# Performance work log

Hardware: AMD Instinct MI355X
Metric: run time of the kernel (lower is better)

## Reference

```python
import jax, jax.numpy as jnp
import numpy as np
from jax import lax

D_MODEL = 384
D_INNER = 768   # expand * d_model
D_STATE = 16
DT_RANK = 24
K_CONV = 4
B_SZ = 2
L_SEQ = 2048


def setup_inputs() -> dict:
    key = jax.random.key(0)
    ks = jax.random.split(key, 11)
    inp = {}
    inp["x"] = jax.random.normal(ks[0], (B_SZ, L_SEQ, D_MODEL), dtype=jnp.float32)
    # learned parameters (Mamba block)
    inp["in_proj_w"] = jax.random.normal(ks[1], (D_MODEL, 2 * D_INNER), dtype=jnp.float32) * 0.02
    inp["conv_w"] = jax.random.normal(ks[2], (D_INNER, K_CONV), dtype=jnp.float32) * 0.1
    inp["conv_b"] = jnp.zeros((D_INNER,), dtype=jnp.float32)
    inp["x_proj_w"] = jax.random.normal(ks[3], (D_INNER, DT_RANK + 2 * D_STATE), dtype=jnp.float32) * 0.02
    inp["dt_proj_w"] = jax.random.normal(ks[4], (DT_RANK, D_INNER), dtype=jnp.float32) * 0.1
    inp["dt_proj_b"] = jnp.full((D_INNER,), -2.0, dtype=jnp.float32)  # softplus(-2) ~ small init dt
    # A_log initialized so A = -exp(A_log) = -[1..d_state]
    inp["A_log"] = jnp.log(jnp.broadcast_to(jnp.arange(1, D_STATE + 1, dtype=jnp.float32), (D_INNER, D_STATE)))
    inp["D"] = jnp.ones((D_INNER,), dtype=jnp.float32)
    inp["out_proj_w"] = jax.random.normal(ks[5], (D_INNER, D_MODEL), dtype=jnp.float32) * 0.02
    return inp


def _silu(x):
    return x * jax.nn.sigmoid(x)


def reference(x, in_proj_w, conv_w, conv_b, x_proj_w, dt_proj_w, dt_proj_b, A_log, D, out_proj_w):
    B, L, _ = x.shape
    d_inner, n = A_log.shape
    k = conv_w.shape[-1]

    # input projection and gate split
    xz = jnp.einsum("bld,de->ble", x, in_proj_w)          # [B, L, 2*d_inner]
    xp, z = jnp.split(xz, 2, axis=-1)                       # each [B, L, d_inner]

    # causal depthwise 1D conv along sequence
    xp_t = xp.transpose(0, 2, 1)                            # [B, d_inner, L]
    conv_out = lax.conv_general_dilated(
        xp_t, conv_w[:, None, :],                           # kernel [O=d_inner, I/g=1, K]
        window_strides=(1,), padding=[(k - 1, 0)],
        dimension_numbers=("NCH", "OIH", "NCH"),
        feature_group_count=d_inner,
    ) + conv_b[None, :, None]
    xp = _silu(conv_out.transpose(0, 2, 1))                 # [B, L, d_inner]

    # data-dependent SSM parameters
    x_dbl = jnp.einsum("bld,de->ble", xp, x_proj_w)         # [B, L, dt_rank + 2n]
    dt_r = x_dbl[..., :DT_RANK]
    Bm = x_dbl[..., DT_RANK:DT_RANK + n]                    # [B, L, n]
    Cm = x_dbl[..., DT_RANK + n:]                           # [B, L, n]
    dt = jax.nn.softplus(jnp.einsum("blr,rd->bld", dt_r, dt_proj_w) + dt_proj_b)  # [B, L, d_inner]

    A = -jnp.exp(A_log)                                     # [d_inner, n]
    dA = jnp.exp(jnp.einsum("bld,dn->bldn", dt, A))         # discretized state transition
    dBx = jnp.einsum("bln,bld->bldn", Bm, dt * xp)          # input contribution

    # sequential selective scan over L
    def step(h, inputs):
        dA_t, dBx_t, C_t = inputs                           # [B,d,n],[B,d,n],[B,n]
        h = dA_t * h + dBx_t
        y = jnp.einsum("bdn,bn->bd", h, C_t)
        return h, y

    h0 = jnp.zeros((B, d_inner, n), dtype=x.dtype)
    _, ys = lax.scan(step, h0, (dA.transpose(1, 0, 2, 3), dBx.transpose(1, 0, 2, 3), Cm.transpose(1, 0, 2)))
    y = ys.transpose(1, 0, 2)                               # [B, L, d_inner]

    y = y + xp * D                                          # skip term
    y = y * _silu(z)                                        # gating
    return jnp.einsum("bld,de->ble", y, out_proj_w)         # [B, L, d_model]
```

## Files before the change

kernel.cpp:

```cpp
#include <hip/hip_runtime.h>
#include <hip/hip_bf16.h>

#define B_SZ    2
#define L_SEQ   2048
#define D_MODEL 384
#define D_INNER 768
#define D_STATE 16
#define DT_RANK 24
#define ML      (B_SZ * L_SEQ)
#define NCHUNK  64
#define CHLEN   (L_SEQ / NCHUNK)

typedef __hip_bfloat16 bf16;
typedef __attribute__((ext_vector_type(8))) short bf16x8;
typedef __attribute__((ext_vector_type(4))) float f32x4;
typedef __attribute__((ext_vector_type(8))) float f32x8;

template<int EPI, int AMODE>
__global__ __launch_bounds__(256)
void gemm_mfma(const float* __restrict__ Af, const bf16* __restrict__ At,
               const float* __restrict__ W,
               bf16* __restrict__ outb0, bf16* __restrict__ outb1,
               float* __restrict__ outf, int M, int N, int K)
{
    __shared__ __attribute__((aligned(16))) short As[64][72];
    __shared__ __attribute__((aligned(16))) short Bs[64][72];
    const int tid  = threadIdx.x;
    const int lane = tid & 63;
    const int wave = tid >> 6;
    const int wm   = (wave & 1) * 32;
    const int wn   = (wave >> 1) * 32;
    const int m0   = blockIdx.y * 64;
    const int n0   = blockIdx.x * 64;

    f32x4 acc[2][2];
#pragma unroll
    for (int i = 0; i < 2; i++)
#pragma unroll
        for (int j = 0; j < 2; j++)
#pragma unroll
            for (int r = 0; r < 4; r++) acc[i][j][r] = 0.f;

    for (int kt = 0; kt < K; kt += 64) {
        __syncthreads();
#pragma unroll
        for (int i = 0; i < 2; i++) {
            int c = tid + 256 * i;
            if (AMODE == 0) {
                int m = c >> 3, k8 = (c & 7) * 8;
                f32x8 a = *(const f32x8*)&Af[(size_t)(m0 + m) * K + kt + k8];
                bf16x8 h;
#pragma unroll
                for (int j = 0; j < 8; j++)
                    h[j] = (short)__bfloat16_as_ushort(__float2bfloat16(a[j]));
                *(bf16x8*)&As[m][k8] = h;
            } else {
                int m8 = (c & 7) * 8, k = c >> 3;
                bf16x8 a = *(const bf16x8*)&At[(size_t)(kt + k) * M + m0 + m8];
#pragma unroll
                for (int j = 0; j < 8; j++) As[m8 + j][k] = a[j];
            }
        }
#pragma unroll
        for (int i = 0; i < 2; i++) {
            int c = tid + 256 * i;
            int n8 = (c & 7) * 8, k = c >> 3;
            if (n0 + n8 + 8 <= N) {
                f32x8 w = *(const f32x8*)&W[(size_t)(kt + k) * N + n0 + n8];
#pragma unroll
                for (int j = 0; j < 8; j++)
                    Bs[n8 + j][k] = (short)__bfloat16_as_ushort(__float2bfloat16(w[j]));
            } else {
#pragma unroll
                for (int j = 0; j < 8; j++) Bs[n8 + j][k] = 0;
            }
        }
        __syncthreads();
#pragma unroll
        for (int ks = 0; ks < 2; ks++) {
            int kb = ks * 32 + (lane >> 4) * 8;
            bf16x8 a0 = *(const bf16x8*)&As[wm + (lane & 15)][kb];
            bf16x8 a1 = *(const bf16x8*)&As[wm + 16 + (lane & 15)][kb];
            bf16x8 b0 = *(const bf16x8*)&Bs[wn + (lane & 15)][kb];
            bf16x8 b1 = *(const bf16x8*)&Bs[wn + 16 + (lane & 15)][kb];
            acc[0][0] = __builtin_amdgcn_mfma_f32_16x16x32_bf16(a0, b0, acc[0][0], 0, 0, 0);
            acc[0][1] = __builtin_amdgcn_mfma_f32_16x16x32_bf16(a0, b1, acc[0][1], 0, 0, 0);
            acc[1][0] = __builtin_amdgcn_mfma_f32_16x16x32_bf16(a1, b0, acc[1][0], 0, 0, 0);
            acc[1][1] = __builtin_amdgcn_mfma_f32_16x16x32_bf16(a1, b1, acc[1][1], 0, 0, 0);
        }
    }

#pragma unroll
    for (int am = 0; am < 2; am++)
#pragma unroll
        for (int bn = 0; bn < 2; bn++)
#pragma unroll
            for (int r = 0; r < 4; r++) {
                int m = m0 + wm + am * 16 + (lane >> 4) * 4 + r;
                int n = n0 + wn + bn * 16 + (lane & 15);
                float v = acc[am][bn][r];
                if (EPI == 0) {
                    if (n < D_INNER)
                        outb0[(size_t)n * ML + m] = __float2bfloat16(v);
                    else
                        outb1[(size_t)(n - D_INNER) * ML + m] =
                            __float2bfloat16(v / (1.f + __expf(-v)));
                } else {
                    if (n < N) outf[(size_t)m * N + n] = v;
                }
            }
}

__global__ __launch_bounds__(256)
void gemm_xproj_split(const bf16* __restrict__ At, const float* __restrict__ W,
                      float* __restrict__ outf, int M, int N, int K)
{
    __shared__ __attribute__((aligned(16))) short As[64][72];
    __shared__ __attribute__((aligned(16))) short Bs[64][72];
    const int tid  = threadIdx.x;
    const int lane = tid & 63;
    const int wave = tid >> 6;
    const int wm   = (wave & 1) * 32;
    const int wn   = (wave >> 1) * 32;
    const int m0   = blockIdx.y * 64;
    const int k0   = blockIdx.x * (768 / 4);

    f32x4 acc[2][2];
#pragma unroll
    for (int i = 0; i < 2; i++)
#pragma unroll
        for (int j = 0; j < 2; j++)
#pragma unroll
            for (int r = 0; r < 4; r++) acc[i][j][r] = 0.f;

    for (int kt = k0; kt < k0 + 192; kt += 64) {
        __syncthreads();
#pragma unroll
        for (int i = 0; i < 2; i++) {
            int c = tid + 256 * i;
            int m8 = (c & 7) * 8, k = c >> 3;
            bf16x8 a = *(const bf16x8*)&At[(size_t)(kt + k) * M + m0 + m8];
#pragma unroll
            for (int j = 0; j < 8; j++) As[m8 + j][k] = a[j];
        }
#pragma unroll
        for (int i = 0; i < 2; i++) {
            int c = tid + 256 * i;
            int n8 = (c & 7) * 8, k = c >> 3;
            if (n8 + 8 <= N) {
                f32x8 w = *(const f32x8*)&W[(size_t)(kt + k) * N + n8];
#pragma unroll
                for (int j = 0; j < 8; j++)
                    Bs[n8 + j][k] = (short)__bfloat16_as_ushort(__float2bfloat16(w[j]));
            } else {
#pragma unroll
                for (int j = 0; j < 8; j++) Bs[n8 + j][k] = 0;
            }
        }
        __syncthreads();
#pragma unroll
        for (int ks = 0; ks < 2; ks++) {
            int kb = ks * 32 + (lane >> 4) * 8;
            bf16x8 a0 = *(const bf16x8*)&As[wm + (lane & 15)][kb];
            bf16x8 a1 = *(const bf16x8*)&As[wm + 16 + (lane & 15)][kb];
            bf16x8 b0 = *(const bf16x8*)&Bs[wn + (lane & 15)][kb];
            bf16x8 b1 = *(const bf16x8*)&Bs[wn + 16 + (lane & 15)][kb];
            acc[0][0] = __builtin_amdgcn_mfma_f32_16x16x32_bf16(a0, b0, acc[0][0], 0, 0, 0);
            acc[0][1] = __builtin_amdgcn_mfma_f32_16x16x32_bf16(a0, b1, acc[0][1], 0, 0, 0);
            acc[1][0] = __builtin_amdgcn_mfma_f32_16x16x32_bf16(a1, b0, acc[1][0], 0, 0, 0);
            acc[1][1] = __builtin_amdgcn_mfma_f32_16x16x32_bf16(a1, b1, acc[1][1], 0, 0, 0);
        }
    }

#pragma unroll
    for (int am = 0; am < 2; am++)
#pragma unroll
        for (int bn = 0; bn < 2; bn++)
#pragma unroll
            for (int r = 0; r < 4; r++) {
                int m = m0 + wm + am * 16 + (lane >> 4) * 4 + r;
                int n = wn + bn * 16 + (lane & 15);
                if (n < N)
                    atomicAdd(&outf[(size_t)m * N + n], acc[am][bn][r]);
            }
}

__global__ __launch_bounds__(256)
void conv_silu_kernel(const bf16* __restrict__ xp_raw_t,
                      const float* __restrict__ cw, const float* __restrict__ cb,
                      bf16* __restrict__ xp_t, float* __restrict__ x_dbl_zero)
{
    {
        int gidx = (blockIdx.y * gridDim.x + blockIdx.x) * 256 + threadIdx.x;
        if (gidx < ML * 56) x_dbl_zero[gidx] = 0.f;
    }

    const int ml0 = (blockIdx.x * 256 + threadIdx.x) * 8;
    const int d   = blockIdx.y;
    const int l0  = ml0 & (L_SEQ - 1);
    const size_t row = (size_t)d * ML;
    const float w0 = cw[d * 4 + 0], w1 = cw[d * 4 + 1],
                w2 = cw[d * 4 + 2], w3 = cw[d * 4 + 3], bias = cb[d];

    bf16x8 cur = *(const bf16x8*)&xp_raw_t[row + ml0];
    bf16x8 prev;
    if (ml0 != 0) prev = *(const bf16x8*)&xp_raw_t[row + ml0 - 8];
    else {
#pragma unroll
        for (int j = 0; j < 8; j++) prev[j] = 0;
    }
    float w[16];
#pragma unroll
    for (int k = 0; k < 8; k++) {
        w[k]     = __uint_as_float(((unsigned)(unsigned short)prev[k]) << 16);
        w[k + 8] = __uint_as_float(((unsigned)(unsigned short)cur[k]) << 16);
    }

    bf16x8 out;
#pragma unroll
    for (int o = 0; o < 8; o++) {
        int l = l0 + o;
        float s = bias;
        if (l >= 3) {
            s += w0 * w[5 + o] + w1 * w[6 + o] + w2 * w[7 + o] + w3 * w[8 + o];
        } else {
            if (l - 3 >= 0) s += w0 * w[5 + o];
            if (l - 2 >= 0) s += w1 * w[6 + o];
            if (l - 1 >= 0) s += w2 * w[7 + o];
            s += w3 * w[8 + o];
        }
        float act = s / (1.f + __expf(-s));
        out[o] = (short)__bfloat16_as_ushort(__float2bfloat16(act));
    }
    *(bf16x8*)&xp_t[row + ml0] = out;
}

__global__ __launch_bounds__(256)
void dt_kernel(const float* __restrict__ x_dbl, const float* __restrict__ dtw,
               const float* __restrict__ dtb, bf16* __restrict__ dt_t)
{
    __shared__ float xs[64 * 25];
    __shared__ float ws[24 * 48];
    const int tid = threadIdx.x;
    const int m0 = blockIdx.x * 64;
    const int d0 = blockIdx.y * 48;
#pragma unroll
    for (int i = 0; i < 6; i++) {
        int idx = tid + 256 * i;
        int r_ = idx / 24, cc = idx % 24;
        xs[r_ * 25 + cc] = x_dbl[(size_t)(m0 + r_) * 56 + cc];
    }
#pragma unroll
    for (int i = 0; i < 5; i++) {
        int idx = tid + 256 * i;
        if (idx < 24 * 48) {
            int r_ = idx / 48, dd = idx % 48;
            ws[idx] = dtw[r_ * D_INNER + d0 + dd];
        }
    }
    __syncthreads();
#pragma unroll
    for (int i = 0; i < 12; i++) {
        int o = tid + 256 * i;
        int mloc = o & 63, dd = o >> 6;
        float acc = dtb[d0 + dd];
#pragma unroll
        for (int r_ = 0; r_ < 24; r_++)
            acc += xs[mloc * 25 + r_] * ws[r_ * 48 + dd];
        float sp = fmaxf(acc, 0.f) + log1pf(__expf(-fabsf(acc)));
        dt_t[(size_t)(d0 + dd) * ML + m0 + mloc] = __float2bfloat16(sp);
    }
}

__global__ __launch_bounds__(1024)
void scan_kernel(const bf16* __restrict__ dt_t, const bf16* __restrict__ xp_t,
                 const float* __restrict__ x_dbl, const bf16* __restrict__ zs_t,
                 const float* __restrict__ A_log, const float* __restrict__ Dp,
                 bf16* __restrict__ y_t)
{
    __shared__ float sP[NCHUNK][D_STATE + 1];
    __shared__ float sH[NCHUNK][D_STATE + 1];
    const int tid = threadIdx.x;
    const int c = tid >> 4;
    const int n = tid & 15;
    const int g = blockIdx.x;
    const int b = g / D_INNER;
    const int d = g % D_INNER;
    const float A = -__expf(A_log[d * D_STATE + n]);
    const size_t base_t = (size_t)d * ML + (size_t)b * L_SEQ + (size_t)c * CHLEN;
    const size_t base_m = (size_t)b * L_SEQ + (size_t)c * CHLEN;

    float h = 0.f, P = 1.f;
#pragma unroll
    for (int g2 = 0; g2 < 2; g2++) {
        bf16x8 vdt0 = *(const bf16x8*)&dt_t[base_t + g2 * 16];
        bf16x8 vdt1 = *(const bf16x8*)&dt_t[base_t + g2 * 16 + 8];
        bf16x8 vxp0 = *(const bf16x8*)&xp_t[base_t + g2 * 16];
        bf16x8 vxp1 = *(const bf16x8*)&xp_t[base_t + g2 * 16 + 8];
#pragma unroll
        for (int k = 0; k < 16; k++) {
            const int j = g2 * 16 + k;
            short sdt = (k < 8) ? vdt0[k & 7] : vdt1[k & 7];
            short sxp = (k < 8) ? vxp0[k & 7] : vxp1[k & 7];
            float dtv = __uint_as_float(((unsigned)(unsigned short)sdt) << 16);
            float xpv = __uint_as_float(((unsigned)(unsigned short)sxp) << 16);
            float Bn  = x_dbl[(base_m + j) * 56 + DT_RANK + n];
            float aj = __expf(dtv * A);
            h = aj * h + Bn * (dtv * xpv);
            P *= aj;
        }
    }
    sP[c][n] = P;
    sH[c][n] = h;
    __syncthreads();

    {
        const int wv = tid >> 6;
        const int ln = tid & 63;
        float p = sP[ln][wv];
        float hh = sH[ln][wv];
#pragma unroll
        for (int s = 1; s < NCHUNK; s <<= 1) {
            float p2 = __shfl_up(p, s);
            float h2 = __shfl_up(hh, s);
            if (ln >= s) { hh = p * h2 + hh; p = p * p2; }
        }
        sP[ln][wv] = p;
        sH[ln][wv] = hh;
    }
    __syncthreads();
    const float hinit = (c == 0) ? 0.f : sH[c - 1][n];

    const float Dd = Dp[d];
    h = hinit;
#pragma unroll
    for (int g2 = 0; g2 < 2; g2++) {
        bf16x8 vdt0 = *(const bf16x8*)&dt_t[base_t + g2 * 16];
        bf16x8 vdt1 = *(const bf16x8*)&dt_t[base_t + g2 * 16 + 8];
        bf16x8 vxp0 = *(const bf16x8*)&xp_t[base_t + g2 * 16];
        bf16x8 vxp1 = *(const bf16x8*)&xp_t[base_t + g2 * 16 + 8];
        float ymine = 0.f, xmine = 0.f;
#pragma unroll
        for (int k = 0; k < 16; k++) {
            const int j = g2 * 16 + k;
            short sdt = (k < 8) ? vdt0[k & 7] : vdt1[k & 7];
            short sxp = (k < 8) ? vxp0[k & 7] : vxp1[k & 7];
            float dtv = __uint_as_float(((unsigned)(unsigned short)sdt) << 16);
            float xpv = __uint_as_float(((unsigned)(unsigned short)sxp) << 16);
            float Bn  = x_dbl[(base_m + j) * 56 + DT_RANK + n];
            float aj = __expf(dtv * A);
            h = aj * h + Bn * (dtv * xpv);
            float Cn = x_dbl[(base_m + j) * 56 + DT_RANK + D_STATE + n];
            float yv = h * Cn;
            yv += __shfl_xor(yv, 1);
            yv += __shfl_xor(yv, 2);
            yv += __shfl_xor(yv, 4);
            yv += __shfl_xor(yv, 8);
            ymine = (k == n) ? yv : ymine;
            xmine = (k == n) ? xpv : xmine;
        }
        const int j = g2 * 16 + n;
        float zsv = __bfloat162float(zs_t[base_t + j]);
        y_t[base_t + j] = __float2bfloat16((ymine + xmine * Dd) * zsv);
    }
}

extern "C" void kernel_launch(void* const* d_in, const int* in_sizes, int n_in,
                              void* d_out, int out_size, void* d_ws, size_t ws_size,
                              hipStream_t stream)
{
    const float* x         = (const float*)d_in[0];
    const float* in_proj_w = (const float*)d_in[1];
    const float* conv_w    = (const float*)d_in[2];
    const float* conv_b    = (const float*)d_in[3];
    const float* x_proj_w  = (const float*)d_in[4];
    const float* dt_proj_w = (const float*)d_in[5];
    const float* dt_proj_b = (const float*)d_in[6];
    const float* A_log     = (const float*)d_in[7];
    const float* Dvec      = (const float*)d_in[8];
    const float* out_proj_w= (const float*)d_in[9];

    bf16* xp_raw_t = (bf16*)d_ws;
    bf16* zs_t     = xp_raw_t + (size_t)ML * D_INNER;
    bf16* xp_t     = zs_t     + (size_t)ML * D_INNER;
    bf16* dt_t     = xp_t     + (size_t)ML * D_INNER;
    float* x_dbl   = (float*)(dt_t + (size_t)ML * D_INNER);
    bf16* y_t      = xp_raw_t;

    dim3 blk(256);

    gemm_mfma<0, 0><<<dim3(2 * D_INNER / 64, ML / 64), blk, 0, stream>>>(
        x, nullptr, in_proj_w, xp_raw_t, zs_t, nullptr, ML, 2 * D_INNER, D_MODEL);

    conv_silu_kernel<<<dim3(ML / 2048, D_INNER), blk, 0, stream>>>(
        xp_raw_t, conv_w, conv_b, xp_t, x_dbl);

    gemm_xproj_split<<<dim3(4, ML / 64), blk, 0, stream>>>(
        xp_t, x_proj_w, x_dbl, ML, 56, D_INNER);

    dt_kernel<<<dim3(ML / 64, D_INNER / 48), blk, 0, stream>>>(
        x_dbl, dt_proj_w, dt_proj_b, dt_t);

    scan_kernel<<<B_SZ * D_INNER, 1024, 0, stream>>>(
        dt_t, xp_t, x_dbl, zs_t, A_log, Dvec, y_t);

    gemm_mfma<1, 1><<<dim3(D_MODEL / 64, ML / 64), blk, 0, stream>>>(
        nullptr, y_t, out_proj_w, nullptr, nullptr, (float*)d_out, ML, D_MODEL, D_INNER);
}
```

Baseline: 239.8 us.

## Store B/C state-major and reuse first-pass scan results instead of recomputing

The x_proj epilogue now writes dt_rank values to a compact row-major buffer and the B and C columns to a transposed [n][ML] buffer, so the scan can load B and C with contiguous vector loads. The scan's first pass keeps per-step h*C and P*C in registers. The second pass then computes outputs as hC + hinit*(P*C) instead of re-running the recurrence with exp and reloading inputs. This removes the redundant second recurrence and the strided per-element x_dbl loads. In exchange it uses 64 extra registers per thread in a 1024-thread block, which risks spills or lower occupancy.

```diff
diff --git a/kernel.cpp b/kernel.cpp
--- a/kernel.cpp
+++ b/kernel.cpp
@@ -113,7 +113,8 @@
 
 __global__ __launch_bounds__(256)
 void gemm_xproj_split(const bf16* __restrict__ At, const float* __restrict__ W,
-                      float* __restrict__ outf, int M, int N, int K)
+                      float* __restrict__ out_dt, float* __restrict__ out_bc,
+                      int M, int N, int K)
 {
     __shared__ __attribute__((aligned(16))) short As[64][72];
     __shared__ __attribute__((aligned(16))) short Bs[64][72];
@@ -180,8 +181,11 @@
             for (int r = 0; r < 4; r++) {
                 int m = m0 + wm + am * 16 + (lane >> 4) * 4 + r;
                 int n = wn + bn * 16 + (lane & 15);
-                if (n < N)
-                    atomicAdd(&outf[(size_t)m * N + n], acc[am][bn][r]);
+                float v = acc[am][bn][r];
+                if (n < DT_RANK)
+                    atomicAdd(&out_dt[(size_t)m * DT_RANK + n], v);
+                else if (n < DT_RANK + 2 * D_STATE)
+                    atomicAdd(&out_bc[(size_t)(n - DT_RANK) * ML + m], v);
             }
 }
 
@@ -248,7 +252,7 @@
     for (int i = 0; i < 6; i++) {
         int idx = tid + 256 * i;
         int r_ = idx / 24, cc = idx % 24;
-        xs[r_ * 25 + cc] = x_dbl[(size_t)(m0 + r_) * 56 + cc];
+        xs[r_ * 25 + cc] = x_dbl[(size_t)(m0 + r_) * 24 + cc];
     }
 #pragma unroll
     for (int i = 0; i < 5; i++) {
@@ -274,7 +278,7 @@
 
 __global__ __launch_bounds__(1024)
 void scan_kernel(const bf16* __restrict__ dt_t, const bf16* __restrict__ xp_t,
-                 const float* __restrict__ x_dbl, const bf16* __restrict__ zs_t,
+                 const float* __restrict__ bc, const bf16* __restrict__ zs_t,
                  const float* __restrict__ A_log, const float* __restrict__ Dp,
                  bf16* __restrict__ y_t)
 {
@@ -289,25 +293,31 @@
     const float A = -__expf(A_log[d * D_STATE + n]);
     const size_t base_t = (size_t)d * ML + (size_t)b * L_SEQ + (size_t)c * CHLEN;
     const size_t base_m = (size_t)b * L_SEQ + (size_t)c * CHLEN;
-
+    const float* __restrict__ Bp = bc + (size_t)n * ML + base_m;
+    const float* __restrict__ Cp = bc + (size_t)(D_STATE + n) * ML + base_m;
+
+    float hC[CHLEN], sc[CHLEN];
     float h = 0.f, P = 1.f;
 #pragma unroll
-    for (int g2 = 0; g2 < 2; g2++) {
-        bf16x8 vdt0 = *(const bf16x8*)&dt_t[base_t + g2 * 16];
-        bf16x8 vdt1 = *(const bf16x8*)&dt_t[base_t + g2 * 16 + 8];
-        bf16x8 vxp0 = *(const bf16x8*)&xp_t[base_t + g2 * 16];
-        bf16x8 vxp1 = *(const bf16x8*)&xp_t[base_t + g2 * 16 + 8];
-#pragma unroll
-        for (int k = 0; k < 16; k++) {
-            const int j = g2 * 16 + k;
-            short sdt = (k < 8) ? vdt0[k & 7] : vdt1[k & 7];
-            short sxp = (k < 8) ? vxp0[k & 7] : vxp1[k & 7];
-            float dtv = __uint_as_float(((unsigned)(unsigned short)sdt) << 16);
-            float xpv = __uint_as_float(((unsigned)(unsigned short)sxp) << 16);
-            float Bn  = x_dbl[(base_m + j) * 56 + DT_RANK + n];
+    for (int q = 0; q < 4; q++) {
+        bf16x8 vdt = *(const bf16x8*)&dt_t[base_t + q * 8];
+        bf16x8 vxp = *(const bf16x8*)&xp_t[base_t + q * 8];
+        f32x4 b0 = *(const f32x4*)&Bp[q * 8];
+        f32x4 b1 = *(const f32x4*)&Bp[q * 8 + 4];
+        f32x4 c0 = *(const f32x4*)&Cp[q * 8];
+        f32x4 c1 = *(const f32x4*)&Cp[q * 8 + 4];
+#pragma unroll
+        for (int k = 0; k < 8; k++) {
+            const int j = q * 8 + k;
+            float dtv = __uint_as_float(((unsigned)(unsigned short)vdt[k]) << 16);
+            float xpv = __uint_as_float(((unsigned)(unsigned short)vxp[k]) << 16);
+            float Bn  = (k < 4) ? b0[k & 3] : b1[k & 3];
+            float Cn  = (k < 4) ? c0[k & 3] : c1[k & 3];
             float aj = __expf(dtv * A);
             h = aj * h + Bn * (dtv * xpv);
             P *= aj;
+            hC[j] = h * Cn;
+            sc[j] = P * Cn;
         }
     }
     sP[c][n] = P;
@@ -332,36 +342,23 @@
     const float hinit = (c == 0) ? 0.f : sH[c - 1][n];
 
     const float Dd = Dp[d];
-    h = hinit;
 #pragma unroll
     for (int g2 = 0; g2 < 2; g2++) {
-        bf16x8 vdt0 = *(const bf16x8*)&dt_t[base_t + g2 * 16];
-        bf16x8 vdt1 = *(const bf16x8*)&dt_t[base_t + g2 * 16 + 8];
-        bf16x8 vxp0 = *(const bf16x8*)&xp_t[base_t + g2 * 16];
-        bf16x8 vxp1 = *(const bf16x8*)&xp_t[base_t + g2 * 16 + 8];
-        float ymine = 0.f, xmine = 0.f;
+        float ymine = 0.f;
 #pragma unroll
         for (int k = 0; k < 16; k++) {
             const int j = g2 * 16 + k;
-            short sdt = (k < 8) ? vdt0[k & 7] : vdt1[k & 7];
-            short sxp = (k < 8) ? vxp0[k & 7] : vxp1[k & 7];
-            float dtv = __uint_as_float(((unsigned)(unsigned short)sdt) << 16);
-            float xpv = __uint_as_float(((unsigned)(unsigned short)sxp) << 16);
-            float Bn  = x_dbl[(base_m + j) * 56 + DT_RANK + n];
-            float aj = __expf(dtv * A);
-            h = aj * h + Bn * (dtv * xpv);
-            float Cn = x_dbl[(base_m + j) * 56 + DT_RANK + D_STATE + n];
-            float yv = h * Cn;
-            yv += __shfl_xor(yv, 1);
-            yv += __shfl_xor(yv, 2);
-            yv += __shfl_xor(yv, 4);
-            yv += __shfl_xor(yv, 8);
-            ymine = (k == n) ? yv : ymine;
-            xmine = (k == n) ? xpv : xmine;
+            float v = hC[j] + hinit * sc[j];
+            v += __shfl_xor(v, 1);
+            v += __shfl_xor(v, 2);
+            v += __shfl_xor(v, 4);
+            v += __shfl_xor(v, 8);
+            ymine = (k == n) ? v : ymine;
         }
         const int j = g2 * 16 + n;
+        float xpv = __bfloat162float(xp_t[base_t + j]);
         float zsv = __bfloat162float(zs_t[base_t + j]);
-        y_t[base_t + j] = __float2bfloat16((ymine + xmine * Dd) * zsv);
+        y_t[base_t + j] = __float2bfloat16((ymine + xpv * Dd) * zsv);
     }
 }
 
@@ -385,6 +382,7 @@
     bf16* xp_t     = zs_t     + (size_t)ML * D_INNER;
     bf16* dt_t     = xp_t     + (size_t)ML * D_INNER;
     float* x_dbl   = (float*)(dt_t + (size_t)ML * D_INNER);
+    float* bc      = x_dbl + (size_t)ML * DT_RANK;
     bf16* y_t      = xp_raw_t;
 
     dim3 blk(256);
@@ -396,13 +394,13 @@
         xp_raw_t, conv_w, conv_b, xp_t, x_dbl);
 
     gemm_xproj_split<<<dim3(4, ML / 64), blk, 0, stream>>>(
-        xp_t, x_proj_w, x_dbl, ML, 56, D_INNER);
+        xp_t, x_proj_w, x_dbl, bc, ML, 56, D_INNER);
 
     dt_kernel<<<dim3(ML / 64, D_INNER / 48), blk, 0, stream>>>(
         x_dbl, dt_proj_w, dt_proj_b, dt_t);
 
     scan_kernel<<<B_SZ * D_INNER, 1024, 0, stream>>>(
-        dt_t, xp_t, x_dbl, zs_t, A_log, Dvec, y_t);
+        dt_t, xp_t, bc, zs_t, A_log, Dvec, y_t);
 
     gemm_mfma<1, 1><<<dim3(D_MODEL / 64, ML / 64), blk, 0, stream>>>(
         nullptr, y_t, out_proj_w, nullptr, nullptr, (float*)d_out, ML, D_MODEL, D_INNER);
```

Measured after the change: 268.3 us. 1.12x slower.
